# Kernel optimization log

Hardware: AMD Instinct MI355X
Metric: run time of the kernel (lower is better)

## Reference

```python
import jax, jax.numpy as jnp
import numpy as np

N, C, B = 800000, 64, 8
BN_EPS = 1e-5


def setup_inputs() -> dict:
    key = jax.random.key(0)
    ks = jax.random.split(key, 8)
    x = jax.random.normal(ks[0], (N, C), dtype=jnp.float32)
    # cumulative end-offsets of B equal segments: [100000, 200000, ..., 800000]
    o = (jnp.arange(1, B + 1, dtype=jnp.int64) * (N // B))
    s2 = 1.0 / np.sqrt(C)
    s1 = 1.0 / np.sqrt(2 * C)
    w2 = jax.random.uniform(ks[1], (C, C), jnp.float32, -s2, s2)      # linear2 Linear(C,C)
    b2 = jax.random.uniform(ks[2], (C,), jnp.float32, -s2, s2)
    w1 = jax.random.uniform(ks[3], (C, 2 * C), jnp.float32, -s1, s1)  # linear1 Linear(2C,C)
    b1 = jax.random.uniform(ks[4], (C,), jnp.float32, -s1, s1)
    gamma = jnp.ones((C,), jnp.float32)   # BatchNorm1d weight
    beta = jnp.zeros((C,), jnp.float32)   # BatchNorm1d bias
    return {"x": x, "o": o, "w2": w2, "b2": b2, "w1": w1, "b1": b1,
            "gamma": gamma, "beta": beta}


def reference(x, o, w2, b2, w1, b1, gamma, beta):
    n = x.shape[0]
    nb = o.shape[0]
    # segment id of each point: point i belongs to segment j iff o[j-1] <= i < o[j]
    seg = jnp.searchsorted(o, jnp.arange(n), side="right")          # [N]
    counts = jnp.diff(o, prepend=0).astype(x.dtype)                  # [B]
    # per-segment mean pool
    means = jax.ops.segment_sum(x, seg, num_segments=nb) / counts[:, None]  # [B, C]
    # linear2: Linear + ReLU on pooled vectors
    h = jax.nn.relu(means @ w2.T + b2)                               # [B, C]
    # broadcast pooled features back to points and concat
    cat = jnp.concatenate([x, h[seg]], axis=1)                       # [N, 2C]
    # linear1: Linear + BatchNorm1d (training-mode batch stats) + ReLU
    y = cat @ w1.T + b1                                              # [N, C]
    mu = y.mean(axis=0)
    var = y.var(axis=0)
    y = (y - mu) * jax.lax.rsqrt(var + BN_EPS) * gamma + beta
    return jax.nn.relu(y)
```

## Files before the change

### kernel.cpp

```cpp
#include <hip/hip_runtime.h>

#define NROWS 800000
#define SEGROWS 100000
#define K1_BLOCKS 800
#define K1_ROWS 1000

typedef __attribute__((ext_vector_type(8))) short bf16x8;
typedef __attribute__((ext_vector_type(4))) float f32x4;
typedef __attribute__((ext_vector_type(4))) short short4v;

__device__ inline unsigned short f2bf(float f) {
    unsigned u = __builtin_bit_cast(unsigned, f);
    return (unsigned short)((u + 0x7FFFu + ((u >> 16) & 1u)) >> 16);
}

__global__ void kzero(float* __restrict__ p) {
    int t = blockIdx.x * 256 + threadIdx.x;
    if (t < 4608) p[t] = 0.f;
}

__global__ __launch_bounds__(256, 2)
void k1_stats(const float* __restrict__ x, float* __restrict__ m2g, float* __restrict__ ssumg)
{
    __shared__ __align__(16) float smem[5120];
    short* xt = (short*)smem;
    const float4* X4 = (const float4*)x;
    int t = threadIdx.x, w = t >> 6, lane = t & 63;
    int c4 = t & 15, g = t >> 4;
    size_t r0 = (size_t)blockIdx.x * K1_ROWS;
    int seg = (int)(r0 / SEGROWS);

    f32x4 acc[4][4];
#pragma unroll
    for (int p = 0; p < 4; ++p)
#pragma unroll
        for (int q = 0; q < 4; ++q) acc[p][q] = (f32x4){0.f, 0.f, 0.f, 0.f};
    float s0 = 0, s1 = 0, s2 = 0, s3 = 0;

    for (int tile = 0; tile < K1_ROWS; tile += 128) {
        int nr = min(128, K1_ROWS - tile);
        __syncthreads();
#pragma unroll
        for (int h = 0; h < 2; ++h) {
            int rg = 8 * g + 4 * h;
            float4 v[4];
#pragma unroll
            for (int i = 0; i < 4; ++i) {
                int r = rg + i;
                if (r < nr) {
                    v[i] = X4[(r0 + tile + r) * 16 + c4];
                    s0 += v[i].x; s1 += v[i].y; s2 += v[i].z; s3 += v[i].w;
                } else v[i] = make_float4(0.f, 0.f, 0.f, 0.f);
            }
#pragma unroll
            for (int j = 0; j < 4; ++j) {
                short4v pk;
                pk[0] = (short)f2bf(((const float*)&v[0])[j]);
                pk[1] = (short)f2bf(((const float*)&v[1])[j]);
                pk[2] = (short)f2bf(((const float*)&v[2])[j]);
                pk[3] = (short)f2bf(((const float*)&v[3])[j]);
                *(short4v*)&xt[(4 * c4 + j) * 136 + rg] = pk;
            }
        }
        __syncthreads();
        bf16x8 f[4];
#pragma unroll
        for (int c0 = 0; c0 < 4; ++c0)
            f[c0] = *(const bf16x8*)&xt[(16 * c0 + (lane & 15)) * 136 + 32 * w + 8 * (lane >> 4)];
#pragma unroll
        for (int p = 0; p < 4; ++p)
#pragma unroll
            for (int q = 0; q < 4; ++q)
                acc[p][q] = __builtin_amdgcn_mfma_f32_16x16x32_bf16(f[p], f[q], acc[p][q], 0, 0, 0);
    }

    __syncthreads();
    ((float4*)(smem + 4096))[t] = make_float4(s0, s1, s2, s3);
    int qd = lane >> 4, cl = lane & 15;
    if (w == 0) {
#pragma unroll
        for (int p = 0; p < 4; ++p)
#pragma unroll
            for (int q = 0; q < 4; ++q)
#pragma unroll
                for (int i = 0; i < 4; ++i)
                    smem[(16 * p + 4 * qd + i) * 64 + 16 * q + cl] = acc[p][q][i];
    }
    __syncthreads();
    if (t < 64) {
        int cc4 = t >> 2, ii = t & 3;
        float s = 0;
#pragma unroll
        for (int u = 0; u < 16; ++u) s += smem[4096 + 4 * (cc4 + 16 * u) + ii];
        atomicAdd(&ssumg[seg * 64 + t], s);
    }
    for (int ww = 1; ww < 4; ++ww) {
        if (w == ww) {
#pragma unroll
            for (int p = 0; p < 4; ++p)
#pragma unroll
                for (int q = 0; q < 4; ++q)
#pragma unroll
                    for (int i = 0; i < 4; ++i)
                        smem[(16 * p + 4 * qd + i) * 64 + 16 * q + cl] += acc[p][q][i];
        }
        __syncthreads();
    }
    for (int f2 = t; f2 < 4096; f2 += 256) atomicAdd(&m2g[f2], smem[f2]);
}

__global__ __launch_bounds__(256)
void k2b_solve(const int* __restrict__ o,
               const float* __restrict__ w2, const float* __restrict__ b2,
               const float* __restrict__ w1, const float* __restrict__ b1,
               const float* __restrict__ gamma, const float* __restrict__ beta,
               const float* __restrict__ m2, const float* __restrict__ ssum,
               unsigned short* __restrict__ wpb, float* __restrict__ tbout)
{
    __shared__ float means[512], hb[512], cv[512], Sx[64], cnts[8], muS[64], sS[64], q1p[256];
    int t = threadIdx.x;
    if (t < 8) cnts[t] = (float)(o[t] - (t ? o[t - 1] : 0));
    __syncthreads();
    for (int i = t; i < 512; i += 256) means[i] = ssum[i] / cnts[i >> 6];
    __syncthreads();
    int c = t & 63, g = t >> 6;
    for (int b = g; b < 8; b += 4) {
        float a = b2[c];
        for (int k = 0; k < 64; ++k) a = fmaf(means[b * 64 + k], w2[c * 64 + k], a);
        hb[b * 64 + c] = fmaxf(a, 0.f);
    }
    __syncthreads();
    for (int b = g; b < 8; b += 4) {
        float a = b1[c];
        for (int k = 0; k < 64; ++k) a = fmaf(hb[b * 64 + k], w1[c * 128 + 64 + k], a);
        cv[b * 64 + c] = a;
    }
    __syncthreads();
    if (t < 64) {
        float s = 0;
        for (int b = 0; b < 8; ++b) s += ssum[b * 64 + t];
        Sx[t] = s;
    }
    __syncthreads();
    {
        float p = 0;
        for (int j = g * 16; j < g * 16 + 16; ++j) {
            float vj = 0;
            for (int k = 0; k < 64; ++k) vj = fmaf(w1[c * 128 + k], m2[j * 64 + k], vj);
            p = fmaf(w1[c * 128 + j], vj, p);
        }
        q1p[g * 64 + c] = p;
    }
    __syncthreads();
    if (t < 64) {
        const float Nf = (float)NROWS;
        float mu = 0;
        for (int k = 0; k < 64; ++k) mu = fmaf(w1[t * 128 + k], Sx[k], mu);
        float q2 = 0, q3 = 0, msum = 0;
        for (int b = 0; b < 8; ++b) {
            float gv = cv[b * 64 + t];
            msum += cnts[b] * gv;
            q3 = fmaf(cnts[b] * gv, gv, q3);
            float dot = 0;
            for (int k = 0; k < 64; ++k) dot = fmaf(w1[t * 128 + k], ssum[b * 64 + k], dot);
            q2 = fmaf(2.f * gv, dot, q2);
        }
        mu = (mu + msum) / Nf;
        float q1 = q1p[t] + q1p[64 + t] + q1p[128 + t] + q1p[192 + t];
        float var = (q1 + q2 + q3) / Nf - mu * mu;
        float s = gamma[t] * rsqrtf(var + 1e-5f);
        muS[t] = mu; sS[t] = s;
    }
    __syncthreads();
    for (int f = t; f < 4096; f += 256)
        wpb[f] = f2bf(w1[(f >> 6) * 128 + (f & 63)] * sS[f >> 6]);
    for (int f = t; f < 512; f += 256)
        tbout[f] = (cv[f] - muS[f & 63]) * sS[f & 63] + beta[f & 63];
}

__global__ __launch_bounds__(256, 3)
void k3_gemm(const float* __restrict__ x, const unsigned short* __restrict__ wpb,
             const float* __restrict__ tb, float* __restrict__ out)
{
    __shared__ __align__(16) short bt[64 * 72];
    __shared__ float tbs[512];
    int t = threadIdx.x, lane = t & 63, w = t >> 6;
    size_t r0 = (size_t)blockIdx.x * 256;

    for (int f = t; f < 512; f += 256) {
        int c = f >> 3, kg = f & 7;
        uint4 vv = ((const uint4*)wpb)[f];
        *(uint4*)&bt[c * 72 + kg * 8] = vv;
    }
    for (int f = t; f < 512; f += 256) tbs[f] = tb[f];
    __syncthreads();

    int cl = lane & 15, qd = lane >> 4;
    bf16x8 B[4][2];
#pragma unroll
    for (int n = 0; n < 4; ++n)
#pragma unroll
        for (int k0 = 0; k0 < 2; ++k0)
            B[n][k0] = *(const bf16x8*)&bt[(16 * n + cl) * 72 + 32 * k0 + 8 * qd];

    int rbase = (int)r0 + 64 * w;
    f32x4 acc[4][4];
#pragma unroll
    for (int m = 0; m < 4; ++m)
#pragma unroll
        for (int n = 0; n < 4; ++n) acc[m][n] = (f32x4){0.f, 0.f, 0.f, 0.f};

#pragma unroll
    for (int m = 0; m < 4; ++m) {
        const float* rp = x + (size_t)(rbase + 16 * m + cl) * 64 + 8 * qd;
        float4 u0 = *(const float4*)(rp);
        float4 u1 = *(const float4*)(rp + 4);
        float4 u2 = *(const float4*)(rp + 32);
        float4 u3 = *(const float4*)(rp + 36);
        bf16x8 A0, A1;
        A0[0] = (short)f2bf(u0.x); A0[1] = (short)f2bf(u0.y);
        A0[2] = (short)f2bf(u0.z); A0[3] = (short)f2bf(u0.w);
        A0[4] = (short)f2bf(u1.x); A0[5] = (short)f2bf(u1.y);
        A0[6] = (short)f2bf(u1.z); A0[7] = (short)f2bf(u1.w);
        A1[0] = (short)f2bf(u2.x); A1[1] = (short)f2bf(u2.y);
        A1[2] = (short)f2bf(u2.z); A1[3] = (short)f2bf(u2.w);
        A1[4] = (short)f2bf(u3.x); A1[5] = (short)f2bf(u3.y);
        A1[6] = (short)f2bf(u3.z); A1[7] = (short)f2bf(u3.w);
#pragma unroll
        for (int n = 0; n < 4; ++n) {
            acc[m][n] = __builtin_amdgcn_mfma_f32_16x16x32_bf16(A0, B[n][0], acc[m][n], 0, 0, 0);
            acc[m][n] = __builtin_amdgcn_mfma_f32_16x16x32_bf16(A1, B[n][1], acc[m][n], 0, 0, 0);
        }
    }

    int seg0 = rbase / SEGROWS;
    int bnd = (seg0 + 1) * SEGROWS;
    int seg1 = min(seg0 + 1, 7);
    float tA[4], tB[4];
#pragma unroll
    for (int n = 0; n < 4; ++n) {
        tA[n] = tbs[seg0 * 64 + 16 * n + cl];
        tB[n] = tbs[seg1 * 64 + 16 * n + cl];
    }
#pragma unroll
    for (int m = 0; m < 4; ++m)
#pragma unroll
        for (int i = 0; i < 4; ++i) {
            int grow = rbase + 16 * m + 4 * qd + i;
            bool hi = grow >= bnd;
#pragma unroll
            for (int n = 0; n < 4; ++n) {
                float tv = hi ? tB[n] : tA[n];
                float vv = fmaxf(acc[m][n][i] + tv, 0.f);
                out[(size_t)grow * 64 + 16 * n + cl] = vv;
            }
        }
}

extern "C" void kernel_launch(void* const* d_in, const int* in_sizes, int n_in,
                              void* d_out, int out_size, void* d_ws, size_t ws_size,
                              hipStream_t stream)
{
    const float* x  = (const float*)d_in[0];
    const int*   o  = (const int*)d_in[1];
    const float* w2 = (const float*)d_in[2];
    const float* b2 = (const float*)d_in[3];
    const float* w1 = (const float*)d_in[4];
    const float* b1 = (const float*)d_in[5];
    const float* gm = (const float*)d_in[6];
    const float* bt = (const float*)d_in[7];
    float* out = (float*)d_out;
    float* ws  = (float*)d_ws;

    float*          m2g  = ws;
    float*          ssum = ws + 4096;
    float*          tbv  = ws + 4608;
    unsigned short* wpb  = (unsigned short*)(ws + 5120);

    kzero<<<18, 256, 0, stream>>>(ws);
    k1_stats<<<K1_BLOCKS, 256, 0, stream>>>(x, m2g, ssum);
    k2b_solve<<<1, 256, 0, stream>>>(o, w2, b2, w1, b1, gm, bt, m2g, ssum, wpb, tbv);
    k3_gemm<<<3125, 256, 0, stream>>>(x, wpb, tbv, out);
}
```

Baseline: 472.3 us.

## Fuse stats solve into GEMM kernel and rebalance stats work per segment

The single-block solve kernel is merged into the GEMM kernel: each of 625 persistent blocks recomputes the BN statistics and the folded bf16 weights redundantly, then processes five 256-row chunks. This removes a serialized one-block launch and the workspace round-trip for the weights and bias. The stats kernel now uses 512 blocks, 64 per segment, striding over 128-row tiles, and staggers its final atomic adds across blocks to reduce contention. The cost is redundant per-block solve work (several 64x64 dot loops reading w1 and m2 from global memory) and fewer, longer GEMM blocks.

```diff
diff --git a/kernel.cpp b/kernel.cpp
--- a/kernel.cpp
+++ b/kernel.cpp
@@ -2,8 +2,9 @@
 
 #define NROWS 800000
 #define SEGROWS 100000
-#define K1_BLOCKS 800
-#define K1_ROWS 1000
+#define TPS 782
+#define K1_BLOCKS 512
+#define K23_BLOCKS 625
 
 typedef __attribute__((ext_vector_type(8))) short bf16x8;
 typedef __attribute__((ext_vector_type(4))) float f32x4;
@@ -27,8 +28,7 @@
     const float4* X4 = (const float4*)x;
     int t = threadIdx.x, w = t >> 6, lane = t & 63;
     int c4 = t & 15, g = t >> 4;
-    size_t r0 = (size_t)blockIdx.x * K1_ROWS;
-    int seg = (int)(r0 / SEGROWS);
+    const int seg = blockIdx.x >> 6, jj = blockIdx.x & 63;
 
     f32x4 acc[4][4];
 #pragma unroll
@@ -37,8 +37,9 @@
         for (int q = 0; q < 4; ++q) acc[p][q] = (f32x4){0.f, 0.f, 0.f, 0.f};
     float s0 = 0, s1 = 0, s2 = 0, s3 = 0;
 
-    for (int tile = 0; tile < K1_ROWS; tile += 128) {
-        int nr = min(128, K1_ROWS - tile);
+    for (int tl = jj; tl < TPS; tl += 64) {
+        const size_t r0 = (size_t)seg * SEGROWS + (size_t)tl * 128;
+        const int nr = (tl == TPS - 1) ? 32 : 128;
         __syncthreads();
 #pragma unroll
         for (int h = 0; h < 2; ++h) {
@@ -48,7 +49,7 @@
             for (int i = 0; i < 4; ++i) {
                 int r = rg + i;
                 if (r < nr) {
-                    v[i] = X4[(r0 + tile + r) * 16 + c4];
+                    v[i] = X4[(r0 + r) * 16 + c4];
                     s0 += v[i].x; s1 += v[i].y; s2 += v[i].z; s3 += v[i].w;
                 } else v[i] = make_float4(0.f, 0.f, 0.f, 0.f);
             }
@@ -106,155 +107,153 @@
         }
         __syncthreads();
     }
-    for (int f2 = t; f2 < 4096; f2 += 256) atomicAdd(&m2g[f2], smem[f2]);
-}
-
-__global__ __launch_bounds__(256)
-void k2b_solve(const int* __restrict__ o,
-               const float* __restrict__ w2, const float* __restrict__ b2,
-               const float* __restrict__ w1, const float* __restrict__ b1,
-               const float* __restrict__ gamma, const float* __restrict__ beta,
-               const float* __restrict__ m2, const float* __restrict__ ssum,
-               unsigned short* __restrict__ wpb, float* __restrict__ tbout)
+#pragma unroll
+    for (int ii = 0; ii < 16; ++ii) {
+        int f2 = t + 256 * ((ii + blockIdx.x) & 15);
+        atomicAdd(&m2g[f2], smem[f2]);
+    }
+}
+
+__global__ __launch_bounds__(256, 3)
+void k23(const float* __restrict__ x, const int* __restrict__ o,
+         const float* __restrict__ w2, const float* __restrict__ b2,
+         const float* __restrict__ w1, const float* __restrict__ b1,
+         const float* __restrict__ gamma, const float* __restrict__ beta,
+         const float* __restrict__ m2, const float* __restrict__ ssum,
+         float* __restrict__ out)
 {
-    __shared__ float means[512], hb[512], cv[512], Sx[64], cnts[8], muS[64], sS[64], q1p[256];
-    int t = threadIdx.x;
-    if (t < 8) cnts[t] = (float)(o[t] - (t ? o[t - 1] : 0));
-    __syncthreads();
-    for (int i = t; i < 512; i += 256) means[i] = ssum[i] / cnts[i >> 6];
-    __syncthreads();
-    int c = t & 63, g = t >> 6;
-    for (int b = g; b < 8; b += 4) {
-        float a = b2[c];
-        for (int k = 0; k < 64; ++k) a = fmaf(means[b * 64 + k], w2[c * 64 + k], a);
-        hb[b * 64 + c] = fmaxf(a, 0.f);
-    }
-    __syncthreads();
-    for (int b = g; b < 8; b += 4) {
-        float a = b1[c];
-        for (int k = 0; k < 64; ++k) a = fmaf(hb[b * 64 + k], w1[c * 128 + 64 + k], a);
-        cv[b * 64 + c] = a;
-    }
-    __syncthreads();
-    if (t < 64) {
-        float s = 0;
-        for (int b = 0; b < 8; ++b) s += ssum[b * 64 + t];
-        Sx[t] = s;
-    }
-    __syncthreads();
-    {
-        float p = 0;
-        for (int j = g * 16; j < g * 16 + 16; ++j) {
-            float vj = 0;
-            for (int k = 0; k < 64; ++k) vj = fmaf(w1[c * 128 + k], m2[j * 64 + k], vj);
-            p = fmaf(w1[c * 128 + j], vj, p);
-        }
-        q1p[g * 64 + c] = p;
-    }
-    __syncthreads();
-    if (t < 64) {
-        const float Nf = (float)NROWS;
-        float mu = 0;
-        for (int k = 0; k < 64; ++k) mu = fmaf(w1[t * 128 + k], Sx[k], mu);
-        float q2 = 0, q3 = 0, msum = 0;
-        for (int b = 0; b < 8; ++b) {
-            float gv = cv[b * 64 + t];
-            msum += cnts[b] * gv;
-            q3 = fmaf(cnts[b] * gv, gv, q3);
-            float dot = 0;
-            for (int k = 0; k < 64; ++k) dot = fmaf(w1[t * 128 + k], ssum[b * 64 + k], dot);
-            q2 = fmaf(2.f * gv, dot, q2);
-        }
-        mu = (mu + msum) / Nf;
-        float q1 = q1p[t] + q1p[64 + t] + q1p[128 + t] + q1p[192 + t];
-        float var = (q1 + q2 + q3) / Nf - mu * mu;
-        float s = gamma[t] * rsqrtf(var + 1e-5f);
-        muS[t] = mu; sS[t] = s;
-    }
-    __syncthreads();
-    for (int f = t; f < 4096; f += 256)
-        wpb[f] = f2bf(w1[(f >> 6) * 128 + (f & 63)] * sS[f >> 6]);
-    for (int f = t; f < 512; f += 256)
-        tbout[f] = (cv[f] - muS[f & 63]) * sS[f & 63] + beta[f & 63];
-}
-
-__global__ __launch_bounds__(256, 3)
-void k3_gemm(const float* __restrict__ x, const unsigned short* __restrict__ wpb,
-             const float* __restrict__ tb, float* __restrict__ out)
-{
+    __shared__ float means[512], hb[512], cv[512], q1p[256];
+    __shared__ float Sx[64], muS[64], sS[64], cnts[8];
     __shared__ __align__(16) short bt[64 * 72];
     __shared__ float tbs[512];
-    int t = threadIdx.x, lane = t & 63, w = t >> 6;
-    size_t r0 = (size_t)blockIdx.x * 256;
-
-    for (int f = t; f < 512; f += 256) {
-        int c = f >> 3, kg = f & 7;
-        uint4 vv = ((const uint4*)wpb)[f];
-        *(uint4*)&bt[c * 72 + kg * 8] = vv;
-    }
-    for (int f = t; f < 512; f += 256) tbs[f] = tb[f];
-    __syncthreads();
-
-    int cl = lane & 15, qd = lane >> 4;
-    bf16x8 B[4][2];
-#pragma unroll
-    for (int n = 0; n < 4; ++n)
-#pragma unroll
-        for (int k0 = 0; k0 < 2; ++k0)
-            B[n][k0] = *(const bf16x8*)&bt[(16 * n + cl) * 72 + 32 * k0 + 8 * qd];
-
-    int rbase = (int)r0 + 64 * w;
-    f32x4 acc[4][4];
-#pragma unroll
-    for (int m = 0; m < 4; ++m)
-#pragma unroll
-        for (int n = 0; n < 4; ++n) acc[m][n] = (f32x4){0.f, 0.f, 0.f, 0.f};
-
-#pragma unroll
-    for (int m = 0; m < 4; ++m) {
-        const float* rp = x + (size_t)(rbase + 16 * m + cl) * 64 + 8 * qd;
-        float4 u0 = *(const float4*)(rp);
-        float4 u1 = *(const float4*)(rp + 4);
-        float4 u2 = *(const float4*)(rp + 32);
-        float4 u3 = *(const float4*)(rp + 36);
-        bf16x8 A0, A1;
-        A0[0] = (short)f2bf(u0.x); A0[1] = (short)f2bf(u0.y);
-        A0[2] = (short)f2bf(u0.z); A0[3] = (short)f2bf(u0.w);
-        A0[4] = (short)f2bf(u1.x); A0[5] = (short)f2bf(u1.y);
-        A0[6] = (short)f2bf(u1.z); A0[7] = (short)f2bf(u1.w);
-        A1[0] = (short)f2bf(u2.x); A1[1] = (short)f2bf(u2.y);
-        A1[2] = (short)f2bf(u2.z); A1[3] = (short)f2bf(u2.w);
-        A1[4] = (short)f2bf(u3.x); A1[5] = (short)f2bf(u3.y);
-        A1[6] = (short)f2bf(u3.z); A1[7] = (short)f2bf(u3.w);
-#pragma unroll
-        for (int n = 0; n < 4; ++n) {
-            acc[m][n] = __builtin_amdgcn_mfma_f32_16x16x32_bf16(A0, B[n][0], acc[m][n], 0, 0, 0);
-            acc[m][n] = __builtin_amdgcn_mfma_f32_16x16x32_bf16(A1, B[n][1], acc[m][n], 0, 0, 0);
-        }
-    }
-
-    int seg0 = rbase / SEGROWS;
-    int bnd = (seg0 + 1) * SEGROWS;
-    int seg1 = min(seg0 + 1, 7);
-    float tA[4], tB[4];
-#pragma unroll
-    for (int n = 0; n < 4; ++n) {
-        tA[n] = tbs[seg0 * 64 + 16 * n + cl];
-        tB[n] = tbs[seg1 * 64 + 16 * n + cl];
-    }
-#pragma unroll
-    for (int m = 0; m < 4; ++m)
-#pragma unroll
-        for (int i = 0; i < 4; ++i) {
-            int grow = rbase + 16 * m + 4 * qd + i;
-            bool hi = grow >= bnd;
+
+    const int t = threadIdx.x, lane = t & 63, w = t >> 6;
+
+    {
+        if (t < 8) cnts[t] = (float)(o[t] - (t ? o[t - 1] : 0));
+        __syncthreads();
+        for (int i = t; i < 512; i += 256) means[i] = ssum[i] / cnts[i >> 6];
+        __syncthreads();
+        const int c = t & 63, g = t >> 6;
+        for (int b = g; b < 8; b += 4) {
+            float a = b2[c];
+            for (int k = 0; k < 64; ++k) a = fmaf(means[b * 64 + k], w2[c * 64 + k], a);
+            hb[b * 64 + c] = fmaxf(a, 0.f);
+        }
+        __syncthreads();
+        for (int b = g; b < 8; b += 4) {
+            float a = b1[c];
+            for (int k = 0; k < 64; ++k) a = fmaf(hb[b * 64 + k], w1[c * 128 + 64 + k], a);
+            cv[b * 64 + c] = a;
+        }
+        __syncthreads();
+        if (t < 64) {
+            float s = 0;
+            for (int b = 0; b < 8; ++b) s += ssum[b * 64 + t];
+            Sx[t] = s;
+        }
+        __syncthreads();
+        {
+            float p = 0;
+            for (int j = g * 16; j < g * 16 + 16; ++j) {
+                float vj = 0;
+                for (int k = 0; k < 64; ++k) vj = fmaf(w1[c * 128 + k], m2[j * 64 + k], vj);
+                p = fmaf(w1[c * 128 + j], vj, p);
+            }
+            q1p[g * 64 + c] = p;
+        }
+        __syncthreads();
+        if (t < 64) {
+            const float Nf = (float)NROWS;
+            float mu = 0;
+            for (int k = 0; k < 64; ++k) mu = fmaf(w1[t * 128 + k], Sx[k], mu);
+            float q2 = 0, q3 = 0, msum = 0;
+            for (int b = 0; b < 8; ++b) {
+                float gv = cv[b * 64 + t];
+                msum += cnts[b] * gv;
+                q3 = fmaf(cnts[b] * gv, gv, q3);
+                float dot = 0;
+                for (int k = 0; k < 64; ++k) dot = fmaf(w1[t * 128 + k], ssum[b * 64 + k], dot);
+                q2 = fmaf(2.f * gv, dot, q2);
+            }
+            mu = (mu + msum) / Nf;
+            float q1 = q1p[t] + q1p[64 + t] + q1p[128 + t] + q1p[192 + t];
+            float var = (q1 + q2 + q3) / Nf - mu * mu;
+            float s = gamma[t] * rsqrtf(var + 1e-5f);
+            muS[t] = mu; sS[t] = s;
+        }
+        __syncthreads();
+        for (int f = t; f < 4096; f += 256)
+            bt[(f >> 6) * 72 + (f & 63)] = (short)f2bf(w1[(f >> 6) * 128 + (f & 63)] * sS[f >> 6]);
+        for (int f = t; f < 512; f += 256)
+            tbs[f] = (cv[f] - muS[f & 63]) * sS[f & 63] + beta[f & 63];
+        __syncthreads();
+    }
+
+    {
+        const int cl = lane & 15, qd = lane >> 4;
+        bf16x8 B[4][2];
+#pragma unroll
+        for (int n = 0; n < 4; ++n)
+#pragma unroll
+            for (int k0 = 0; k0 < 2; ++k0)
+                B[n][k0] = *(const bf16x8*)&bt[(16 * n + cl) * 72 + 32 * k0 + 8 * qd];
+
+        for (int chunk = blockIdx.x * 5; chunk < blockIdx.x * 5 + 5; ++chunk) {
+            const int rbase = chunk * 256 + 64 * w;
+            f32x4 acc[4][4];
+#pragma unroll
+            for (int m = 0; m < 4; ++m)
+#pragma unroll
+                for (int n = 0; n < 4; ++n) acc[m][n] = (f32x4){0.f, 0.f, 0.f, 0.f};
+
+#pragma unroll
+            for (int m = 0; m < 4; ++m) {
+                const float* rp = x + (size_t)(rbase + 16 * m + cl) * 64 + 8 * qd;
+                float4 u0 = *(const float4*)(rp);
+                float4 u1 = *(const float4*)(rp + 4);
+                float4 u2 = *(const float4*)(rp + 32);
+                float4 u3 = *(const float4*)(rp + 36);
+                bf16x8 A0, A1;
+                A0[0] = (short)f2bf(u0.x); A0[1] = (short)f2bf(u0.y);
+                A0[2] = (short)f2bf(u0.z); A0[3] = (short)f2bf(u0.w);
+                A0[4] = (short)f2bf(u1.x); A0[5] = (short)f2bf(u1.y);
+                A0[6] = (short)f2bf(u1.z); A0[7] = (short)f2bf(u1.w);
+                A1[0] = (short)f2bf(u2.x); A1[1] = (short)f2bf(u2.y);
+                A1[2] = (short)f2bf(u2.z); A1[3] = (short)f2bf(u2.w);
+                A1[4] = (short)f2bf(u3.x); A1[5] = (short)f2bf(u3.y);
+                A1[6] = (short)f2bf(u3.z); A1[7] = (short)f2bf(u3.w);
+#pragma unroll
+                for (int n = 0; n < 4; ++n) {
+                    acc[m][n] = __builtin_amdgcn_mfma_f32_16x16x32_bf16(A0, B[n][0], acc[m][n], 0, 0, 0);
+                    acc[m][n] = __builtin_amdgcn_mfma_f32_16x16x32_bf16(A1, B[n][1], acc[m][n], 0, 0, 0);
+                }
+            }
+
+            const int seg0 = rbase / SEGROWS;
+            const int bnd = (seg0 + 1) * SEGROWS;
+            const int seg1 = min(seg0 + 1, 7);
+            float tA[4], tB[4];
 #pragma unroll
             for (int n = 0; n < 4; ++n) {
-                float tv = hi ? tB[n] : tA[n];
-                float vv = fmaxf(acc[m][n][i] + tv, 0.f);
-                out[(size_t)grow * 64 + 16 * n + cl] = vv;
-            }
-        }
+                tA[n] = tbs[seg0 * 64 + 16 * n + cl];
+                tB[n] = tbs[seg1 * 64 + 16 * n + cl];
+            }
+#pragma unroll
+            for (int m = 0; m < 4; ++m)
+#pragma unroll
+                for (int i = 0; i < 4; ++i) {
+                    int grow = rbase + 16 * m + 4 * qd + i;
+                    bool hi = grow >= bnd;
+#pragma unroll
+                    for (int n = 0; n < 4; ++n) {
+                        float tv = hi ? tB[n] : tA[n];
+                        float vv = fmaxf(acc[m][n][i] + tv, 0.f);
+                        out[(size_t)grow * 64 + 16 * n + cl] = vv;
+                    }
+                }
+        }
+    }
 }
 
 extern "C" void kernel_launch(void* const* d_in, const int* in_sizes, int n_in,
@@ -272,13 +271,10 @@
     float* out = (float*)d_out;
     float* ws  = (float*)d_ws;
 
-    float*          m2g  = ws;
-    float*          ssum = ws + 4096;
-    float*          tbv  = ws + 4608;
-    unsigned short* wpb  = (unsigned short*)(ws + 5120);
+    float* m2g  = ws;
+    float* ssum = ws + 4096;
 
     kzero<<<18, 256, 0, stream>>>(ws);
     k1_stats<<<K1_BLOCKS, 256, 0, stream>>>(x, m2g, ssum);
-    k2b_solve<<<1, 256, 0, stream>>>(o, w2, b2, w1, b1, gm, bt, m2g, ssum, wpb, tbv);
-    k3_gemm<<<3125, 256, 0, stream>>>(x, wpb, tbv, out);
-}
+    k23<<<K23_BLOCKS, 256, 0, stream>>>(x, o, w2, b2, w1, b1, gm, bt, m2g, ssum, out);
+}
```

After: 573.1 us. 1.21x slower.
